# Kernel optimization log

Hardware: AMD Instinct MI355X
Metric: run time of the kernel (lower is better)

Reference implementation:

```python
import jax, jax.numpy as jnp
import numpy as np


def setup_inputs() -> dict:
    key = jax.random.key(0)
    k1, k2 = jax.random.split(key)
    B, P, N, M = 8, 32, 1024, 1024
    normalized_receptive_fields = jax.random.normal(k1, (B, P, N, 3), dtype=jnp.float32)
    reconstructed_points = jax.random.normal(k2, (B, P, M, 3), dtype=jnp.float32)
    return {
        "normalized_receptive_fields": normalized_receptive_fields,
        "reconstructed_points": reconstructed_points,
    }


def reference(normalized_receptive_fields, reconstructed_points):
    B, P, M, _ = reconstructed_points.shape
    N = normalized_receptive_fields.shape[2]
    # Faithful to torch: permute(0,1,3,2) then reshape(-1, M, 3).
    x = jnp.transpose(reconstructed_points, (0, 1, 3, 2)).reshape(-1, M, 3)  # (BP, M, 3)
    y = normalized_receptive_fields.reshape(-1, N, 3)                        # (BP, N, 3)
    xx = jnp.sum(x * x, axis=-1)                 # (BP, M)
    yy = jnp.sum(y * y, axis=-1)                 # (BP, N)
    xy = jnp.einsum('bmc,bnc->bmn', x, y)        # (BP, M, N)
    dist = xx[:, :, None] + yy[:, None, :] - 2.0 * xy  # (BP, M, N)
    min_x_to_y = jnp.min(dist, axis=2)           # (BP, M)
    min_y_to_x = jnp.min(dist, axis=1)           # (BP, N)
    return jnp.mean(min_x_to_y) + jnp.mean(min_y_to_x)
```

## Files before the change

### kernel.cpp

```cpp
#include <hip/hip_runtime.h>
#include <hip/hip_bf16.h>


#define MM 1024
#define NN 1024
#define THREADS 1024
#define NWAVES (THREADS / 64)
#define ROWS_PER_WAVE (MM / NWAVES)
#define RB 4
#define CPL (NN / 64)
#define FINF 3.4e38f

__global__ __launch_bounds__(THREADS, 4)
void chamfer_kernel(const float* __restrict__ nrf,
                    const float* __restrict__ rp,
                    float* __restrict__ out,
                    float inv_bpm, float inv_bpn) {
    const int bp   = blockIdx.x;
    const int tid  = threadIdx.x;
    const int lane = tid & 63;
    const int wave = tid >> 6;

    __shared__ float  rpS[MM * 3];
    __shared__ float4 xS[MM];
    __shared__ float  colminS[NWAVES][NN];
    __shared__ float  rowsumS[NWAVES];
    __shared__ float  csumS[NWAVES];

    const float* rpB = rp  + (size_t)bp * MM * 3;
    const float* yB  = nrf + (size_t)bp * NN * 3;

    for (int i = tid; i < MM * 3; i += THREADS) rpS[i] = rpB[i];

    float y0[CPL], y1[CPL], y2[CPL], yy[CPL], colmin[CPL];
    #pragma unroll
    for (int i = 0; i < CPL; ++i) {
        int n = i * 64 + lane;
        float a = yB[n * 3 + 0];
        float b = yB[n * 3 + 1];
        float c = yB[n * 3 + 2];
        y0[i] = a; y1[i] = b; y2[i] = c;
        yy[i] = a * a + b * b + c * c;
        colmin[i] = FINF;
    }
    __syncthreads();

    {
        const int k = 3 * tid;
        float a = rpS[((k + 0) & (MM - 1)) * 3 + ((k + 0) >> 10)];
        float b = rpS[((k + 1) & (MM - 1)) * 3 + ((k + 1) >> 10)];
        float c = rpS[((k + 2) & (MM - 1)) * 3 + ((k + 2) >> 10)];
        xS[tid] = make_float4(-2.0f * a, -2.0f * b, -2.0f * c,
                              a * a + b * b + c * c);
    }
    __syncthreads();

    float rowsum = 0.0f;
    const int m0 = wave * ROWS_PER_WAVE;
    for (int r0 = 0; r0 < ROWS_PER_WAVE; r0 += RB) {
        float4 x[RB];
        #pragma unroll
        for (int j = 0; j < RB; ++j) x[j] = xS[m0 + r0 + j];

        float rmin[RB];
        #pragma unroll
        for (int j = 0; j < RB; ++j) rmin[j] = FINF;

        #pragma unroll
        for (int i = 0; i < CPL; ++i) {
            const float a = y0[i], b = y1[i], c = y2[i], s = yy[i];
            float e[RB];
            #pragma unroll
            for (int j = 0; j < RB; ++j) {
                e[j] = __builtin_fmaf(x[j].x, a,
                        __builtin_fmaf(x[j].y, b,
                         __builtin_fmaf(x[j].z, c, s)));
                rmin[j] = fminf(rmin[j], e[j]);
            }
            float d01 = fminf(e[0] + x[0].w, e[1] + x[1].w);
            float d23 = fminf(e[2] + x[2].w, e[3] + x[3].w);
            colmin[i] = fminf(colmin[i], fminf(d01, d23));
        }

        #pragma unroll
        for (int off = 32; off > 0; off >>= 1) {
            #pragma unroll
            for (int j = 0; j < RB; ++j)
                rmin[j] = fminf(rmin[j], __shfl_xor(rmin[j], off, 64));
        }
        #pragma unroll
        for (int j = 0; j < RB; ++j) rowsum += x[j].w + rmin[j];
    }

    #pragma unroll
    for (int i = 0; i < CPL; ++i) colminS[wave][i * 64 + lane] = colmin[i];
    if (lane == 0) rowsumS[wave] = rowsum;
    __syncthreads();

    {
        const int n = tid;
        float cm = colminS[0][n];
        #pragma unroll
        for (int w = 1; w < NWAVES; ++w) cm = fminf(cm, colminS[w][n]);
        float csum = cm;
        #pragma unroll
        for (int off = 32; off > 0; off >>= 1)
            csum += __shfl_xor(csum, off, 64);
        if (lane == 0) csumS[wave] = csum;
    }
    __syncthreads();

    if (tid == 0) {
        float rs = 0.0f, cs = 0.0f;
        #pragma unroll
        for (int w = 0; w < NWAVES; ++w) { rs += rowsumS[w]; cs += csumS[w]; }
        atomicAdd(out, rs * inv_bpm + cs * inv_bpn);
    }
}

extern "C" void kernel_launch(void* const* d_in, const int* in_sizes, int n_in,
                              void* d_out, int out_size, void* d_ws, size_t ws_size,
                              hipStream_t stream) {
    const float* nrf = (const float*)d_in[0];
    const float* rp  = (const float*)d_in[1];
    float* out = (float*)d_out;

    const int BP = in_sizes[1] / (MM * 3);
    const float inv_bpm = 1.0f / (float)(BP * MM);
    const float inv_bpn = 1.0f / (float)(BP * NN);

    hipMemsetAsync(out, 0, sizeof(float), stream);
    chamfer_kernel<<<BP, THREADS, 0, stream>>>(nrf, rp, out, inv_bpm, inv_bpn);
}
```

Before: 98.24 us.

## Split columns across wave pairs to halve per-thread register arrays

Each wave now owns half of the N columns (8 per lane instead of 16) and a 128-row group shared with a partner wave, so the per-thread y/colmin register arrays are halved. Per-row partial minima are written to shared memory and merged across the two half-column waves in the epilogue, and the column reduction now spans only the 8 waves that cover each half. This is meant to cut register pressure and raise occupancy under the 1024-thread launch bound. The cost is extra shared-memory traffic for the row partials and, per wave, shorter inner loops relative to the shuffle reductions.

```diff
diff --git a/kernel.cpp b/kernel.cpp
--- a/kernel.cpp
+++ b/kernel.cpp
@@ -5,10 +5,11 @@
 #define MM 1024
 #define NN 1024
 #define THREADS 1024
-#define NWAVES (THREADS / 64)
-#define ROWS_PER_WAVE (MM / NWAVES)
+#define NWAVES 16
+#define HALF 512
+#define CPL 8
 #define RB 4
-#define CPL (NN / 64)
+#define RPG 128
 #define FINF 3.4e38f
 
 __global__ __launch_bounds__(THREADS, 4)
@@ -20,12 +21,14 @@
     const int tid  = threadIdx.x;
     const int lane = tid & 63;
     const int wave = tid >> 6;
+    const int h    = wave & 1;
+    const int g    = wave >> 1;
 
     __shared__ float  rpS[MM * 3];
     __shared__ float4 xS[MM];
-    __shared__ float  colminS[NWAVES][NN];
-    __shared__ float  rowsumS[NWAVES];
-    __shared__ float  csumS[NWAVES];
+    __shared__ float  colminS[NWAVES][HALF];
+    __shared__ float  rowminP[NWAVES][RPG];
+    __shared__ float  partialS[NWAVES];
 
     const float* rpB = rp  + (size_t)bp * MM * 3;
     const float* yB  = nrf + (size_t)bp * NN * 3;
@@ -35,7 +38,7 @@
     float y0[CPL], y1[CPL], y2[CPL], yy[CPL], colmin[CPL];
     #pragma unroll
     for (int i = 0; i < CPL; ++i) {
-        int n = i * 64 + lane;
+        int n = h * HALF + i * 64 + lane;
         float a = yB[n * 3 + 0];
         float b = yB[n * 3 + 1];
         float c = yB[n * 3 + 2];
@@ -55,9 +58,8 @@
     }
     __syncthreads();
 
-    float rowsum = 0.0f;
-    const int m0 = wave * ROWS_PER_WAVE;
-    for (int r0 = 0; r0 < ROWS_PER_WAVE; r0 += RB) {
+    const int m0 = g * RPG;
+    for (int r0 = 0; r0 < RPG; r0 += RB) {
         float4 x[RB];
         #pragma unroll
         for (int j = 0; j < RB; ++j) x[j] = xS[m0 + r0 + j];
@@ -79,7 +81,7 @@
             }
             float d01 = fminf(e[0] + x[0].w, e[1] + x[1].w);
             float d23 = fminf(e[2] + x[2].w, e[3] + x[3].w);
-            colmin[i] = fminf(colmin[i], fminf(d01, d23));
+            colmin[i] = fminf(fminf(colmin[i], d01), d23);
         }
 
         #pragma unroll
@@ -88,33 +90,38 @@
             for (int j = 0; j < RB; ++j)
                 rmin[j] = fminf(rmin[j], __shfl_xor(rmin[j], off, 64));
         }
-        #pragma unroll
-        for (int j = 0; j < RB; ++j) rowsum += x[j].w + rmin[j];
+        if (lane == 0) {
+            *(float4*)&rowminP[wave][r0] =
+                make_float4(rmin[0], rmin[1], rmin[2], rmin[3]);
+        }
     }
 
     #pragma unroll
     for (int i = 0; i < CPL; ++i) colminS[wave][i * 64 + lane] = colmin[i];
-    if (lane == 0) rowsumS[wave] = rowsum;
     __syncthreads();
 
     {
-        const int n = tid;
-        float cm = colminS[0][n];
+        const int m = tid, gg = m >> 7, r = m & (RPG - 1);
+        float rmin_full = xS[m].w + fminf(rowminP[2 * gg][r], rowminP[2 * gg + 1][r]);
+
+        const int hh = tid >> 9, c = tid & (HALF - 1);
+        float cm = colminS[hh][c];
         #pragma unroll
-        for (int w = 1; w < NWAVES; ++w) cm = fminf(cm, colminS[w][n]);
-        float csum = cm;
+        for (int w = 1; w < 8; ++w) cm = fminf(cm, colminS[hh + 2 * w][c]);
+
+        float val = rmin_full * inv_bpm + cm * inv_bpn;
         #pragma unroll
         for (int off = 32; off > 0; off >>= 1)
-            csum += __shfl_xor(csum, off, 64);
-        if (lane == 0) csumS[wave] = csum;
+            val += __shfl_xor(val, off, 64);
+        if (lane == 0) partialS[wave] = val;
     }
     __syncthreads();
 
     if (tid == 0) {
-        float rs = 0.0f, cs = 0.0f;
+        float s = 0.0f;
         #pragma unroll
-        for (int w = 0; w < NWAVES; ++w) { rs += rowsumS[w]; cs += csumS[w]; }
-        atomicAdd(out, rs * inv_bpm + cs * inv_bpn);
+        for (int w = 0; w < NWAVES; ++w) s += partialS[w];
+        atomicAdd(out, s);
     }
 }
 
```

After: 108.6 us. +10.5%, slower.

## Stage Y points in shared memory and use DPP-based wave min reduction

Applied to the files above, without the earlier changes.

Y coordinates and their squared norms are now held as float4 in shared memory and read inside the inner loop, where before they sat in 64 registers per thread. This lowers register pressure, which may help occupancy, but it adds an LDS read per column chunk on every row block. The row-min butterfly reduction is also replaced with DPP row_ror steps plus ds_swizzle and ds_bpermute, aiming for cheaper cross-lane operations than generic shuffles.

```diff
diff --git a/kernel.cpp b/kernel.cpp
--- a/kernel.cpp
+++ b/kernel.cpp
@@ -5,11 +5,29 @@
 #define MM 1024
 #define NN 1024
 #define THREADS 1024
-#define NWAVES (THREADS / 64)
-#define ROWS_PER_WAVE (MM / NWAVES)
+#define NWAVES 16
+#define ROWS_PER_WAVE 64
 #define RB 4
-#define CPL (NN / 64)
+#define CPL 16
 #define FINF 3.4e38f
+
+template <int CTRL>
+__device__ __forceinline__ float dpp_ror_min(float v) {
+    int vi = __float_as_int(v);
+    int t  = __builtin_amdgcn_update_dpp(vi, vi, CTRL, 0xf, 0xf, true);
+    return fminf(v, __int_as_float(t));
+}
+
+__device__ __forceinline__ float wave_min64(float v, int lane_xor32_addr) {
+    v = dpp_ror_min<0x121>(v);
+    v = dpp_ror_min<0x122>(v);
+    v = dpp_ror_min<0x124>(v);
+    v = dpp_ror_min<0x128>(v);
+    int s = __builtin_amdgcn_ds_swizzle(__float_as_int(v), 0x401F);
+    v = fminf(v, __int_as_float(s));
+    int p = __builtin_amdgcn_ds_bpermute(lane_xor32_addr, __float_as_int(v));
+    return fminf(v, __int_as_float(p));
+}
 
 __global__ __launch_bounds__(THREADS, 4)
 void chamfer_kernel(const float* __restrict__ nrf,
@@ -20,9 +38,11 @@
     const int tid  = threadIdx.x;
     const int lane = tid & 63;
     const int wave = tid >> 6;
+    const int xaddr32 = ((lane ^ 32) << 2);
 
     __shared__ float  rpS[MM * 3];
     __shared__ float4 xS[MM];
+    __shared__ float4 yS[NN];
     __shared__ float  colminS[NWAVES][NN];
     __shared__ float  rowsumS[NWAVES];
     __shared__ float  csumS[NWAVES];
@@ -31,17 +51,11 @@
     const float* yB  = nrf + (size_t)bp * NN * 3;
 
     for (int i = tid; i < MM * 3; i += THREADS) rpS[i] = rpB[i];
-
-    float y0[CPL], y1[CPL], y2[CPL], yy[CPL], colmin[CPL];
-    #pragma unroll
-    for (int i = 0; i < CPL; ++i) {
-        int n = i * 64 + lane;
-        float a = yB[n * 3 + 0];
-        float b = yB[n * 3 + 1];
-        float c = yB[n * 3 + 2];
-        y0[i] = a; y1[i] = b; y2[i] = c;
-        yy[i] = a * a + b * b + c * c;
-        colmin[i] = FINF;
+    {
+        float a = yB[tid * 3 + 0];
+        float b = yB[tid * 3 + 1];
+        float c = yB[tid * 3 + 2];
+        yS[tid] = make_float4(a, b, c, a * a + b * b + c * c);
     }
     __syncthreads();
 
@@ -54,6 +68,10 @@
                               a * a + b * b + c * c);
     }
     __syncthreads();
+
+    float colmin[CPL];
+    #pragma unroll
+    for (int i = 0; i < CPL; ++i) colmin[i] = FINF;
 
     float rowsum = 0.0f;
     const int m0 = wave * ROWS_PER_WAVE;
@@ -68,26 +86,22 @@
 
         #pragma unroll
         for (int i = 0; i < CPL; ++i) {
-            const float a = y0[i], b = y1[i], c = y2[i], s = yy[i];
+            const float4 yv = yS[i * 64 + lane];
             float e[RB];
             #pragma unroll
             for (int j = 0; j < RB; ++j) {
-                e[j] = __builtin_fmaf(x[j].x, a,
-                        __builtin_fmaf(x[j].y, b,
-                         __builtin_fmaf(x[j].z, c, s)));
+                e[j] = __builtin_fmaf(x[j].x, yv.x,
+                        __builtin_fmaf(x[j].y, yv.y,
+                         __builtin_fmaf(x[j].z, yv.z, yv.w)));
                 rmin[j] = fminf(rmin[j], e[j]);
             }
             float d01 = fminf(e[0] + x[0].w, e[1] + x[1].w);
             float d23 = fminf(e[2] + x[2].w, e[3] + x[3].w);
-            colmin[i] = fminf(colmin[i], fminf(d01, d23));
+            colmin[i] = fminf(fminf(colmin[i], d01), d23);
         }
 
         #pragma unroll
-        for (int off = 32; off > 0; off >>= 1) {
-            #pragma unroll
-            for (int j = 0; j < RB; ++j)
-                rmin[j] = fminf(rmin[j], __shfl_xor(rmin[j], off, 64));
-        }
+        for (int j = 0; j < RB; ++j) rmin[j] = wave_min64(rmin[j], xaddr32);
         #pragma unroll
         for (int j = 0; j < RB; ++j) rowsum += x[j].w + rmin[j];
     }
@@ -129,6 +143,6 @@
     const float inv_bpm = 1.0f / (float)(BP * MM);
     const float inv_bpn = 1.0f / (float)(BP * NN);
 
-    hipMemsetAsync(out, 0, sizeof(float), stream);
+    (void)hipMemsetAsync(out, 0, sizeof(float), stream);
     chamfer_kernel<<<BP, THREADS, 0, stream>>>(nrf, rp, out, inv_bpm, inv_bpn);
 }
```

Measured after the change: 97.19 us. About the same (-1.1%).
